# Kernel tuning notes

Measured on AMD Instinct MI355X. Metric: run time of the kernel, lower is better.

## Reference

```python
import jax, jax.numpy as jnp
import numpy as np

MARGIN = 0.3
EPS = 1e-6  # torch TripletMarginLoss pairwise_distance eps


def setup_inputs() -> dict:
    key = jax.random.key(0)
    k1, k2 = jax.random.split(key)
    n, d = 8192, 128
    inputs = jax.random.normal(k1, (n, d), dtype=jnp.float32)
    similarity = jax.random.randint(k2, (n, n), 0, 2, dtype=jnp.int32)
    return {"inputs": inputs, "similarity": similarity}


def reference(inputs, similarity):
    # mask[i, j] = True if j is a positive of anchor i
    mask = similarity != 0                      # (n, n) bool
    maskf = mask.astype(inputs.dtype)
    counts = maskf.sum(axis=1, keepdims=True)   # (n, 1), >0 by construction
    # per-anchor center = mean of its positives (masked mean as a GEMM)
    centers = (maskf @ inputs) / counts         # (n, d)
    # dist[i, j] = ||centers[i] - inputs[j]||_2 via the expansion trick
    # (avoids materializing the (n, n, d) difference tensor of the original)
    c2 = jnp.sum(centers * centers, axis=1)[:, None]
    x2 = jnp.sum(inputs * inputs, axis=1)[None, :]
    d2 = c2 + x2 - 2.0 * (centers @ inputs.T)
    dist = jnp.sqrt(jnp.maximum(d2, 0.0))       # (n, n)
    # dist only feeds argmin in the original (indices carry no grad)
    dist = jax.lax.stop_gradient(dist)
    # hard-negative mining: argmin of dist over negatives of each anchor
    neg_idx = jnp.argmin(jnp.where(mask, jnp.inf, dist), axis=1)  # (n,)
    neg_min = inputs[neg_idx]                   # (n, d)
    # TripletMarginLoss(margin=0.3, p=2): anchor=centers, pos=inputs, neg=neg_min
    d_ap = jnp.linalg.norm(centers - inputs + EPS, axis=1)
    d_an = jnp.linalg.norm(centers - neg_min + EPS, axis=1)
    return jnp.mean(jnp.maximum(d_ap - d_an + MARGIN, 0.0))
```

## Files before the change

kernel.cpp:

```cpp
#include <hip/hip_runtime.h>
#include <stdint.h>

#define NN 8192
#define DD 128

typedef float f32x4 __attribute__((ext_vector_type(4)));
typedef short bf16x8 __attribute__((ext_vector_type(8)));

union B8 { uint32_t u[4]; bf16x8 v; };

__device__ inline uint16_t f2bf(float f) {
  uint32_t u = __builtin_bit_cast(uint32_t, f);
  uint32_t r = (u + 0x7FFFu + ((u >> 16) & 1u)) >> 16;
  return (uint16_t)r;
}

__device__ inline f32x4 mfma16(bf16x8 a, bf16x8 b, f32x4 c) {
  return __builtin_amdgcn_mfma_f32_16x16x32_bf16(a, b, c, 0, 0, 0);
}

__global__ __launch_bounds__(256) void k_prep(const float* __restrict__ inp,
                                              uint16_t* __restrict__ inp_bf,
                                              uint16_t* __restrict__ inpT_bf,
                                              float* __restrict__ x2) {
  __shared__ uint16_t ldsT[128 * 65];
  __shared__ float ldsS[256];
  const int tid = threadIdx.x;
  const int j0 = blockIdx.x * 64;
  const int r = tid >> 2;
  const int dseg = (tid & 3) * 32;
  float ss = 0.f;
#pragma unroll
  for (int it = 0; it < 8; ++it) {
    float4 v = *(const float4*)(inp + (size_t)(j0 + r) * DD + dseg + it * 4);
    ss += v.x * v.x + v.y * v.y + v.z * v.z + v.w * v.w;
    uint16_t b0 = f2bf(v.x), b1 = f2bf(v.y), b2 = f2bf(v.z), b3 = f2bf(v.w);
    *(ushort4*)(inp_bf + (size_t)(j0 + r) * DD + dseg + it * 4) = make_ushort4(b0, b1, b2, b3);
    int d = dseg + it * 4;
    ldsT[(d + 0) * 65 + r] = b0;
    ldsT[(d + 1) * 65 + r] = b1;
    ldsT[(d + 2) * 65 + r] = b2;
    ldsT[(d + 3) * 65 + r] = b3;
  }
  ldsS[tid] = ss;
  __syncthreads();
  if (tid < 64) x2[j0 + tid] = ldsS[tid * 4] + ldsS[tid * 4 + 1] + ldsS[tid * 4 + 2] + ldsS[tid * 4 + 3];
#pragma unroll
  for (int it = 0; it < 32; ++it) {
    int flat = it * 256 + tid;
    int d = flat >> 6, jl = flat & 63;
    inpT_bf[(size_t)d * NN + j0 + jl] = ldsT[d * 65 + jl];
  }
}

__global__ __launch_bounds__(256) void k_bitgen(const int* __restrict__ sim,
                                                uint32_t* __restrict__ bmT,
                                                uint32_t* __restrict__ counts) {
  __shared__ uint32_t ldsW[64 * 64];
  const int tid = threadIdx.x, lane = tid & 63, w = tid >> 6;
  const int m0 = blockIdx.x * 64;
  const int c0 = blockIdx.y * 2048;
#pragma unroll 1
  for (int rr = 0; rr < 16; ++rr) {
    const int rl = rr * 4 + w;
    const int row = m0 + rl;
    const int* p = sim + (size_t)row * NN + c0 + lane;
    int v[32];
#pragma unroll
    for (int s = 0; s < 32; ++s) v[s] = p[s * 64];
    uint32_t cnt = 0;
#pragma unroll
    for (int s = 0; s < 32; ++s) {
      unsigned long long ball = __ballot(v[s] != 0);
      cnt += (uint32_t)__popcll(ball);
      if ((lane & 31) == 0)
        ldsW[(s * 2 + (lane >> 5)) * 64 + rl] = (uint32_t)(ball >> (lane & 32));
    }
    if (lane == 0) atomicAdd(&counts[row], cnt);
  }
  __syncthreads();
#pragma unroll
  for (int it = 0; it < 16; ++it) {
    int idx = it * 256 + tid;
    int kw = idx >> 6, r = idx & 63;
    bmT[(size_t)((c0 >> 5) + kw) * NN + m0 + r] = ldsW[idx];
  }
}

__global__ __launch_bounds__(512) void k_gemm1(const uint16_t* __restrict__ inpT,
                                               const uint32_t* __restrict__ bmT,
                                               float* __restrict__ part) {
  __shared__ __align__(16) uint16_t ldsB[128 * 40];
  __shared__ uint32_t ldsM[128];
  const int tid = threadIdx.x, lane = tid & 63, w = tid >> 6;
  const int col = lane & 15, quad = lane >> 4;
  const int m0 = blockIdx.x * 128;
  const int kb0 = blockIdx.y * 2048;
  const int wm = (w >> 1) * 32, wn = (w & 1) * 64;
  const int dim = tid >> 2, koff = (tid & 3) * 8;
  f32x4 acc[2][4];
  const f32x4 z = {0.f, 0.f, 0.f, 0.f};
#pragma unroll
  for (int r = 0; r < 2; ++r)
#pragma unroll
    for (int c = 0; c < 4; ++c) acc[r][c] = z;

  bf16x8 bpf = *(const bf16x8*)(inpT + (size_t)dim * NN + kb0 + koff);
  uint32_t mpf = (tid < 128) ? bmT[(size_t)(kb0 >> 5) * NN + m0 + tid] : 0u;

  for (int ks = 0; ks < 64; ++ks) {
    const int kb = kb0 + ks * 32;
    __syncthreads();
    *(bf16x8*)(ldsB + dim * 40 + koff) = bpf;
    if (tid < 128) ldsM[tid] = mpf;
    __syncthreads();
    if (ks < 63) {
      bpf = *(const bf16x8*)(inpT + (size_t)dim * NN + kb + 32 + koff);
      if (tid < 128) mpf = bmT[(size_t)((kb + 32) >> 5) * NN + m0 + tid];
    }
    B8 af[2];
#pragma unroll
    for (int rr = 0; rr < 2; ++rr) {
      uint32_t word = ldsM[wm + rr * 16 + col];
      uint32_t b = (word >> (quad * 8)) & 0xFFu;
      uint32_t s = b * 0x8001u;
#pragma unroll
      for (int p = 0; p < 4; ++p) {
        uint32_t t = (s >> (2 * p)) & 0x10001u;
        af[rr].u[p] = t * 0x3F80u;
      }
    }
#pragma unroll
    for (int cc = 0; cc < 4; ++cc) {
      bf16x8 bfr = *(const bf16x8*)(ldsB + (wn + cc * 16 + col) * 40 + quad * 8);
#pragma unroll
      for (int rr = 0; rr < 2; ++rr) acc[rr][cc] = mfma16(af[rr].v, bfr, acc[rr][cc]);
    }
  }
  float* pp = part + (size_t)blockIdx.y * NN * DD;
#pragma unroll
  for (int rr = 0; rr < 2; ++rr)
#pragma unroll
    for (int cc = 0; cc < 4; ++cc)
#pragma unroll
      for (int g = 0; g < 4; ++g)
        pp[(size_t)(m0 + wm + rr * 16 + quad * 4 + g) * DD + wn + cc * 16 + col] = acc[rr][cc][g];
}

__global__ __launch_bounds__(256) void k_reduce(const float* __restrict__ part,
                                                const uint32_t* __restrict__ counts,
                                                float* __restrict__ centers,
                                                uint16_t* __restrict__ cen_bf,
                                                unsigned long long* __restrict__ negkey) {
  const int gid = blockIdx.x * 256 + threadIdx.x;
  if (gid < NN) negkey[gid] = ~0ull;
  const int idx = gid * 4;
  const int row = idx >> 7;
  const float inv = 1.0f / (float)counts[row];
  float4 v = *(const float4*)(part + idx);
#pragma unroll
  for (int s = 1; s < 4; ++s) {
    float4 u = *(const float4*)(part + (size_t)s * NN * DD + idx);
    v.x += u.x; v.y += u.y; v.z += u.z; v.w += u.w;
  }
  v.x *= inv; v.y *= inv; v.z *= inv; v.w *= inv;
  *(float4*)(centers + idx) = v;
  *(ushort4*)(cen_bf + idx) = make_ushort4(f2bf(v.x), f2bf(v.y), f2bf(v.z), f2bf(v.w));
}

__global__ __launch_bounds__(256) void k_argmin(const uint16_t* __restrict__ cen_bf,
                                                const uint16_t* __restrict__ inp_bf,
                                                const uint32_t* __restrict__ bmT,
                                                const float* __restrict__ x2,
                                                unsigned long long* __restrict__ negkey) {
  __shared__ __align__(16) uint16_t ldsB[64 * 136];
  __shared__ uint32_t ldsM[128];
  __shared__ float ldsX[64];
  __shared__ unsigned long long ldsR[64];
  const int tid = threadIdx.x, lane = tid & 63, w = tid >> 6;
  const int col = lane & 15, quad = lane >> 4;
  const int i0 = blockIdx.x * 64;
  const int jbase = blockIdx.y * 2048;
  const int wi = (w >> 1) * 32, wj = (w & 1) * 32;
  bf16x8 af[2][4];
#pragma unroll
  for (int rr = 0; rr < 2; ++rr)
#pragma unroll
    for (int kk = 0; kk < 4; ++kk)
      af[rr][kk] = *(const bf16x8*)(cen_bf + (size_t)(i0 + wi + rr * 16 + col) * DD + kk * 32 + quad * 8);
  if (tid < 64) ldsR[tid] = ~0ull;
  float bestv[2][4];
  uint32_t besti[2][4];
#pragma unroll
  for (int rr = 0; rr < 2; ++rr)
#pragma unroll
    for (int g = 0; g < 4; ++g) { bestv[rr][g] = __builtin_inff(); besti[rr][g] = 0u; }

  const int jl = tid >> 2, doff = (tid & 3) * 32;
  bf16x8 bpf[4];
#pragma unroll
  for (int it = 0; it < 4; ++it)
    bpf[it] = *(const bf16x8*)(inp_bf + (size_t)(jbase + jl) * DD + doff + it * 8);
  uint32_t mpf = (tid < 128) ? bmT[(size_t)((jbase >> 5) + (tid >> 6)) * NN + i0 + (tid & 63)] : 0u;
  float xpf = (tid >= 128 && tid < 192) ? x2[jbase + tid - 128] : 0.f;

  for (int js = 0; js < 32; ++js) {
    const int j0 = jbase + js * 64;
    __syncthreads();
#pragma unroll
    for (int it = 0; it < 4; ++it)
      *(bf16x8*)(ldsB + jl * 136 + doff + it * 8) = bpf[it];
    if (tid < 128) ldsM[tid] = mpf;
    else if (tid < 192) ldsX[tid - 128] = xpf;
    __syncthreads();
    if (js < 31) {
#pragma unroll
      for (int it = 0; it < 4; ++it)
        bpf[it] = *(const bf16x8*)(inp_bf + (size_t)(j0 + 64 + jl) * DD + doff + it * 8);
      if (tid < 128) mpf = bmT[(size_t)(((j0 + 64) >> 5) + (tid >> 6)) * NN + i0 + (tid & 63)];
      else if (tid < 192) xpf = x2[j0 + 64 + tid - 128];
    }
    f32x4 acc[2][2];
    const f32x4 z = {0.f, 0.f, 0.f, 0.f};
    acc[0][0] = z; acc[0][1] = z; acc[1][0] = z; acc[1][1] = z;
#pragma unroll
    for (int kk = 0; kk < 4; ++kk) {
      bf16x8 b0 = *(const bf16x8*)(ldsB + (wj + col) * 136 + kk * 32 + quad * 8);
      bf16x8 b1 = *(const bf16x8*)(ldsB + (wj + 16 + col) * 136 + kk * 32 + quad * 8);
      acc[0][0] = mfma16(af[0][kk], b0, acc[0][0]);
      acc[0][1] = mfma16(af[0][kk], b1, acc[0][1]);
      acc[1][0] = mfma16(af[1][kk], b0, acc[1][0]);
      acc[1][1] = mfma16(af[1][kk], b1, acc[1][1]);
    }
    uint32_t wsel = (w & 1) * 64;
    uint32_t words[2][4];
#pragma unroll
    for (int rr = 0; rr < 2; ++rr)
#pragma unroll
      for (int g = 0; g < 4; ++g) words[rr][g] = ldsM[wsel + wi + rr * 16 + quad * 4 + g];
#pragma unroll
    for (int cc = 0; cc < 2; ++cc) {
      const int jj = wj + cc * 16 + col;
      const float xq = ldsX[jj];
      const uint32_t jg = (uint32_t)(j0 + jj);
      const uint32_t bit = cc * 16 + col;
#pragma unroll
      for (int rr = 0; rr < 2; ++rr)
#pragma unroll
        for (int g = 0; g < 4; ++g) {
          float v = fmaf(-2.0f, acc[rr][cc][g], xq);
          if ((words[rr][g] >> bit) & 1u) v = __builtin_inff();
          if (v < bestv[rr][g]) { bestv[rr][g] = v; besti[rr][g] = jg; }
        }
    }
  }
#pragma unroll
  for (int rr = 0; rr < 2; ++rr)
#pragma unroll
    for (int g = 0; g < 4; ++g) {
      float v = bestv[rr][g];
      uint32_t ix = besti[rr][g];
#pragma unroll
      for (int d = 1; d < 16; d <<= 1) {
        float ov = __shfl_xor(v, d);
        uint32_t oi = (uint32_t)__shfl_xor((int)ix, d);
        if (ov < v || (ov == v && oi < ix)) { v = ov; ix = oi; }
      }
      if (col == 0) {
        uint32_t vb = __builtin_bit_cast(uint32_t, v);
        uint32_t key32 = (vb & 0x80000000u) ? ~vb : (vb | 0x80000000u);
        unsigned long long key = ((unsigned long long)key32 << 32) | (unsigned long long)ix;
        atomicMin(&ldsR[wi + rr * 16 + quad * 4 + g], key);
      }
    }
  __syncthreads();
  if (tid < 64) atomicMin(&negkey[i0 + tid], ldsR[tid]);
}

__global__ __launch_bounds__(256) void k_loss(const float* __restrict__ centers,
                                              const float* __restrict__ inp,
                                              const unsigned long long* __restrict__ negkey,
                                              float* __restrict__ out) {
  __shared__ float lds[4];
  const int tid = threadIdx.x, lane = tid & 63, w = tid >> 6;
  float local = 0.f;
#pragma unroll 1
  for (int a = 0; a < 4; ++a) {
    int i = blockIdx.x * 16 + w * 4 + a;
    float2 c = *(const float2*)(centers + (size_t)i * DD + lane * 2);
    float2 x = *(const float2*)(inp + (size_t)i * DD + lane * 2);
    uint32_t ni = ((uint32_t)(negkey[i] & 0xFFFFFFFFull)) & (NN - 1);
    float2 gv = *(const float2*)(inp + (size_t)ni * DD + lane * 2);
    float e0 = c.x - x.x + 1e-6f, e1 = c.y - x.y + 1e-6f;
    float f0 = c.x - gv.x + 1e-6f, f1 = c.y - gv.y + 1e-6f;
    float dap = e0 * e0 + e1 * e1;
    float dan = f0 * f0 + f1 * f1;
#pragma unroll
    for (int d = 32; d; d >>= 1) {
      dap += __shfl_down(dap, d);
      dan += __shfl_down(dan, d);
    }
    if (lane == 0) local += fmaxf(sqrtf(dap) - sqrtf(dan) + 0.3f, 0.f);
  }
  if (lane == 0) lds[w] = local;
  __syncthreads();
  if (tid == 0) atomicAdd(out, (lds[0] + lds[1] + lds[2] + lds[3]) * (1.0f / 8192.0f));
}

extern "C" void kernel_launch(void* const* d_in, const int* in_sizes, int n_in,
                              void* d_out, int out_size, void* d_ws, size_t ws_size,
                              hipStream_t stream) {
  (void)in_sizes; (void)n_in; (void)ws_size;
  const float* inp = (const float*)d_in[0];
  const int* sim = (const int*)d_in[1];
  float* out = (float*)d_out;
  char* ws = (char*)d_ws;

  uint32_t* bmT     = (uint32_t*)ws;
  float* part       = (float*)(ws + (8u << 20));
  float* centers    = (float*)(ws + (24u << 20));
  uint16_t* inp_bf  = (uint16_t*)(ws + (28u << 20));
  uint16_t* inpT_bf = (uint16_t*)(ws + (30u << 20));
  uint16_t* cen_bf  = (uint16_t*)(ws + (32u << 20));
  float* x2         = (float*)(ws + (34u << 20));
  uint32_t* counts  = (uint32_t*)(ws + (34u << 20) + 32768u);
  unsigned long long* negkey = (unsigned long long*)(ws + (34u << 20) + 65536u);

  hipMemsetAsync(counts, 0, NN * sizeof(uint32_t), stream);
  hipMemsetAsync(out, 0, out_size * sizeof(float), stream);

  k_prep<<<128, 256, 0, stream>>>(inp, inp_bf, inpT_bf, x2);
  k_bitgen<<<dim3(128, 4), 256, 0, stream>>>(sim, bmT, counts);
  k_gemm1<<<dim3(64, 4), 512, 0, stream>>>(inpT_bf, bmT, part);
  k_reduce<<<1024, 256, 0, stream>>>(part, counts, centers, cen_bf, negkey);
  k_argmin<<<dim3(128, 4), 256, 0, stream>>>(cen_bf, inp_bf, bmT, x2, negkey);
  k_loss<<<512, 256, 0, stream>>>(centers, inp, negkey, out);
}
```

Baseline: 455.2 us.

## Pack argmin into 32-bit keys and double split-K grids

The argmin inner loop now forms a single 32-bit key: the float distance biased positive by 512, with low mantissa bits replaced by the column index and the mask bit forced into the sign. A plain unsigned min then replaces the compare/select pairs, and the 64-bit shuffles and atomics become 32-bit. Both GEMM kernels double their grid by halving K/J chunks (8 partials, 256-thread blocks), which adds occupancy but also more partial-sum traffic in the reduce. The key truncates 13 mantissa bits of the distance, so near-ties can choose a different negative than exact argmin.

```diff
diff --git a/kernel.cpp b/kernel.cpp
--- a/kernel.cpp
+++ b/kernel.cpp
@@ -22,7 +22,7 @@
 __global__ __launch_bounds__(256) void k_prep(const float* __restrict__ inp,
                                               uint16_t* __restrict__ inp_bf,
                                               uint16_t* __restrict__ inpT_bf,
-                                              float* __restrict__ x2) {
+                                              float* __restrict__ x2p) {
   __shared__ uint16_t ldsT[128 * 65];
   __shared__ float ldsS[256];
   const int tid = threadIdx.x;
@@ -44,7 +44,8 @@
   }
   ldsS[tid] = ss;
   __syncthreads();
-  if (tid < 64) x2[j0 + tid] = ldsS[tid * 4] + ldsS[tid * 4 + 1] + ldsS[tid * 4 + 2] + ldsS[tid * 4 + 3];
+  if (tid < 64)
+    x2p[j0 + tid] = ldsS[tid * 4] + ldsS[tid * 4 + 1] + ldsS[tid * 4 + 2] + ldsS[tid * 4 + 3] + 512.0f;
 #pragma unroll
   for (int it = 0; it < 32; ++it) {
     int flat = it * 256 + tid;
@@ -87,17 +88,17 @@
   }
 }
 
-__global__ __launch_bounds__(512) void k_gemm1(const uint16_t* __restrict__ inpT,
-                                               const uint32_t* __restrict__ bmT,
-                                               float* __restrict__ part) {
+__global__ __launch_bounds__(256, 4) void k_gemm1(const uint16_t* __restrict__ inpT,
+                                                  const uint32_t* __restrict__ bmT,
+                                                  float* __restrict__ part) {
   __shared__ __align__(16) uint16_t ldsB[128 * 40];
-  __shared__ uint32_t ldsM[128];
+  __shared__ uint32_t ldsM[64];
   const int tid = threadIdx.x, lane = tid & 63, w = tid >> 6;
   const int col = lane & 15, quad = lane >> 4;
-  const int m0 = blockIdx.x * 128;
-  const int kb0 = blockIdx.y * 2048;
+  const int m0 = blockIdx.x * 64;
+  const int kb0 = blockIdx.y * 1024;
   const int wm = (w >> 1) * 32, wn = (w & 1) * 64;
-  const int dim = tid >> 2, koff = (tid & 3) * 8;
+  const int dim = tid >> 1, koff = (tid & 1) * 16;
   f32x4 acc[2][4];
   const f32x4 z = {0.f, 0.f, 0.f, 0.f};
 #pragma unroll
@@ -105,18 +106,21 @@
 #pragma unroll
     for (int c = 0; c < 4; ++c) acc[r][c] = z;
 
-  bf16x8 bpf = *(const bf16x8*)(inpT + (size_t)dim * NN + kb0 + koff);
-  uint32_t mpf = (tid < 128) ? bmT[(size_t)(kb0 >> 5) * NN + m0 + tid] : 0u;
-
-  for (int ks = 0; ks < 64; ++ks) {
+  bf16x8 bpf0 = *(const bf16x8*)(inpT + (size_t)dim * NN + kb0 + koff);
+  bf16x8 bpf1 = *(const bf16x8*)(inpT + (size_t)dim * NN + kb0 + koff + 8);
+  uint32_t mpf = (tid < 64) ? bmT[(size_t)(kb0 >> 5) * NN + m0 + tid] : 0u;
+
+  for (int ks = 0; ks < 32; ++ks) {
     const int kb = kb0 + ks * 32;
     __syncthreads();
-    *(bf16x8*)(ldsB + dim * 40 + koff) = bpf;
-    if (tid < 128) ldsM[tid] = mpf;
+    *(bf16x8*)(ldsB + dim * 40 + koff) = bpf0;
+    *(bf16x8*)(ldsB + dim * 40 + koff + 8) = bpf1;
+    if (tid < 64) ldsM[tid] = mpf;
     __syncthreads();
-    if (ks < 63) {
-      bpf = *(const bf16x8*)(inpT + (size_t)dim * NN + kb + 32 + koff);
-      if (tid < 128) mpf = bmT[(size_t)((kb + 32) >> 5) * NN + m0 + tid];
+    if (ks < 31) {
+      bpf0 = *(const bf16x8*)(inpT + (size_t)dim * NN + kb + 32 + koff);
+      bpf1 = *(const bf16x8*)(inpT + (size_t)dim * NN + kb + 32 + koff + 8);
+      if (tid < 64) mpf = bmT[(size_t)((kb + 32) >> 5) * NN + m0 + tid];
     }
     B8 af[2];
 #pragma unroll
@@ -150,16 +154,14 @@
 __global__ __launch_bounds__(256) void k_reduce(const float* __restrict__ part,
                                                 const uint32_t* __restrict__ counts,
                                                 float* __restrict__ centers,
-                                                uint16_t* __restrict__ cen_bf,
-                                                unsigned long long* __restrict__ negkey) {
+                                                uint16_t* __restrict__ cen_bf) {
   const int gid = blockIdx.x * 256 + threadIdx.x;
-  if (gid < NN) negkey[gid] = ~0ull;
   const int idx = gid * 4;
   const int row = idx >> 7;
   const float inv = 1.0f / (float)counts[row];
   float4 v = *(const float4*)(part + idx);
 #pragma unroll
-  for (int s = 1; s < 4; ++s) {
+  for (int s = 1; s < 8; ++s) {
     float4 u = *(const float4*)(part + (size_t)s * NN * DD + idx);
     v.x += u.x; v.y += u.y; v.z += u.z; v.w += u.w;
   }
@@ -168,19 +170,19 @@
   *(ushort4*)(cen_bf + idx) = make_ushort4(f2bf(v.x), f2bf(v.y), f2bf(v.z), f2bf(v.w));
 }
 
-__global__ __launch_bounds__(256) void k_argmin(const uint16_t* __restrict__ cen_bf,
-                                                const uint16_t* __restrict__ inp_bf,
-                                                const uint32_t* __restrict__ bmT,
-                                                const float* __restrict__ x2,
-                                                unsigned long long* __restrict__ negkey) {
+__global__ __launch_bounds__(256, 4) void k_argmin(const uint16_t* __restrict__ cen_bf,
+                                                   const uint16_t* __restrict__ inp_bf,
+                                                   const uint32_t* __restrict__ bmT,
+                                                   const float* __restrict__ x2p,
+                                                   uint32_t* __restrict__ negkey) {
   __shared__ __align__(16) uint16_t ldsB[64 * 136];
   __shared__ uint32_t ldsM[128];
   __shared__ float ldsX[64];
-  __shared__ unsigned long long ldsR[64];
+  __shared__ uint32_t ldsR[64];
   const int tid = threadIdx.x, lane = tid & 63, w = tid >> 6;
   const int col = lane & 15, quad = lane >> 4;
   const int i0 = blockIdx.x * 64;
-  const int jbase = blockIdx.y * 2048;
+  const int jbase = blockIdx.y * 1024;
   const int wi = (w >> 1) * 32, wj = (w & 1) * 32;
   bf16x8 af[2][4];
 #pragma unroll
@@ -188,13 +190,12 @@
 #pragma unroll
     for (int kk = 0; kk < 4; ++kk)
       af[rr][kk] = *(const bf16x8*)(cen_bf + (size_t)(i0 + wi + rr * 16 + col) * DD + kk * 32 + quad * 8);
-  if (tid < 64) ldsR[tid] = ~0ull;
-  float bestv[2][4];
-  uint32_t besti[2][4];
+  if (tid < 64) ldsR[tid] = 0xFFFFFFFFu;
+  uint32_t best[2][4];
 #pragma unroll
   for (int rr = 0; rr < 2; ++rr)
 #pragma unroll
-    for (int g = 0; g < 4; ++g) { bestv[rr][g] = __builtin_inff(); besti[rr][g] = 0u; }
+    for (int g = 0; g < 4; ++g) best[rr][g] = 0xFFFFFFFFu;
 
   const int jl = tid >> 2, doff = (tid & 3) * 32;
   bf16x8 bpf[4];
@@ -202,9 +203,9 @@
   for (int it = 0; it < 4; ++it)
     bpf[it] = *(const bf16x8*)(inp_bf + (size_t)(jbase + jl) * DD + doff + it * 8);
   uint32_t mpf = (tid < 128) ? bmT[(size_t)((jbase >> 5) + (tid >> 6)) * NN + i0 + (tid & 63)] : 0u;
-  float xpf = (tid >= 128 && tid < 192) ? x2[jbase + tid - 128] : 0.f;
-
-  for (int js = 0; js < 32; ++js) {
+  float xpf = (tid >= 128 && tid < 192) ? x2p[jbase + tid - 128] : 0.f;
+
+  for (int js = 0; js < 16; ++js) {
     const int j0 = jbase + js * 64;
     __syncthreads();
 #pragma unroll
@@ -213,12 +214,12 @@
     if (tid < 128) ldsM[tid] = mpf;
     else if (tid < 192) ldsX[tid - 128] = xpf;
     __syncthreads();
-    if (js < 31) {
+    if (js < 15) {
 #pragma unroll
       for (int it = 0; it < 4; ++it)
         bpf[it] = *(const bf16x8*)(inp_bf + (size_t)(j0 + 64 + jl) * DD + doff + it * 8);
       if (tid < 128) mpf = bmT[(size_t)(((j0 + 64) >> 5) + (tid >> 6)) * NN + i0 + (tid & 63)];
-      else if (tid < 192) xpf = x2[j0 + 64 + tid - 128];
+      else if (tid < 192) xpf = x2p[j0 + 64 + tid - 128];
     }
     f32x4 acc[2][2];
     const f32x4 z = {0.f, 0.f, 0.f, 0.f};
@@ -232,7 +233,7 @@
       acc[1][0] = mfma16(af[1][kk], b0, acc[1][0]);
       acc[1][1] = mfma16(af[1][kk], b1, acc[1][1]);
     }
-    uint32_t wsel = (w & 1) * 64;
+    const uint32_t wsel = (w & 1) * 64;
     uint32_t words[2][4];
 #pragma unroll
     for (int rr = 0; rr < 2; ++rr)
@@ -242,15 +243,17 @@
     for (int cc = 0; cc < 2; ++cc) {
       const int jj = wj + cc * 16 + col;
       const float xq = ldsX[jj];
-      const uint32_t jg = (uint32_t)(j0 + jj);
-      const uint32_t bit = cc * 16 + col;
+      const uint32_t jpre = (uint32_t)(j0 + jj);
+      const int sh = 31 - (cc * 16 + col);
 #pragma unroll
       for (int rr = 0; rr < 2; ++rr)
 #pragma unroll
         for (int g = 0; g < 4; ++g) {
           float v = fmaf(-2.0f, acc[rr][cc][g], xq);
-          if ((words[rr][g] >> bit) & 1u) v = __builtin_inff();
-          if (v < bestv[rr][g]) { bestv[rr][g] = v; besti[rr][g] = jg; }
+          uint32_t u = __builtin_bit_cast(uint32_t, v);
+          uint32_t key = (u & 0xFFFFE000u) | jpre;
+          key |= (words[rr][g] << sh) & 0x80000000u;
+          best[rr][g] = min(best[rr][g], key);
         }
     }
   }
@@ -258,20 +261,13 @@
   for (int rr = 0; rr < 2; ++rr)
 #pragma unroll
     for (int g = 0; g < 4; ++g) {
-      float v = bestv[rr][g];
-      uint32_t ix = besti[rr][g];
+      uint32_t k = best[rr][g];
 #pragma unroll
       for (int d = 1; d < 16; d <<= 1) {
-        float ov = __shfl_xor(v, d);
-        uint32_t oi = (uint32_t)__shfl_xor((int)ix, d);
-        if (ov < v || (ov == v && oi < ix)) { v = ov; ix = oi; }
+        uint32_t o = (uint32_t)__shfl_xor((int)k, d);
+        k = min(k, o);
       }
-      if (col == 0) {
-        uint32_t vb = __builtin_bit_cast(uint32_t, v);
-        uint32_t key32 = (vb & 0x80000000u) ? ~vb : (vb | 0x80000000u);
-        unsigned long long key = ((unsigned long long)key32 << 32) | (unsigned long long)ix;
-        atomicMin(&ldsR[wi + rr * 16 + quad * 4 + g], key);
-      }
+      if (col == 0) atomicMin(&ldsR[wi + rr * 16 + quad * 4 + g], k);
     }
   __syncthreads();
   if (tid < 64) atomicMin(&negkey[i0 + tid], ldsR[tid]);
@@ -279,7 +275,7 @@
 
 __global__ __launch_bounds__(256) void k_loss(const float* __restrict__ centers,
                                               const float* __restrict__ inp,
-                                              const unsigned long long* __restrict__ negkey,
+                                              const uint32_t* __restrict__ negkey,
                                               float* __restrict__ out) {
   __shared__ float lds[4];
   const int tid = threadIdx.x, lane = tid & 63, w = tid >> 6;
@@ -289,7 +285,7 @@
     int i = blockIdx.x * 16 + w * 4 + a;
     float2 c = *(const float2*)(centers + (size_t)i * DD + lane * 2);
     float2 x = *(const float2*)(inp + (size_t)i * DD + lane * 2);
-    uint32_t ni = ((uint32_t)(negkey[i] & 0xFFFFFFFFull)) & (NN - 1);
+    uint32_t ni = negkey[i] & (NN - 1);
     float2 gv = *(const float2*)(inp + (size_t)ni * DD + lane * 2);
     float e0 = c.x - x.x + 1e-6f, e1 = c.y - x.y + 1e-6f;
     float f0 = c.x - gv.x + 1e-6f, f1 = c.y - gv.y + 1e-6f;
@@ -318,21 +314,22 @@
 
   uint32_t* bmT     = (uint32_t*)ws;
   float* part       = (float*)(ws + (8u << 20));
-  float* centers    = (float*)(ws + (24u << 20));
-  uint16_t* inp_bf  = (uint16_t*)(ws + (28u << 20));
-  uint16_t* inpT_bf = (uint16_t*)(ws + (30u << 20));
-  uint16_t* cen_bf  = (uint16_t*)(ws + (32u << 20));
-  float* x2         = (float*)(ws + (34u << 20));
-  uint32_t* counts  = (uint32_t*)(ws + (34u << 20) + 32768u);
-  unsigned long long* negkey = (unsigned long long*)(ws + (34u << 20) + 65536u);
+  float* centers    = (float*)(ws + (40u << 20));
+  uint16_t* inp_bf  = (uint16_t*)(ws + (44u << 20));
+  uint16_t* inpT_bf = (uint16_t*)(ws + (46u << 20));
+  uint16_t* cen_bf  = (uint16_t*)(ws + (48u << 20));
+  float* x2p        = (float*)(ws + (50u << 20));
+  uint32_t* counts  = (uint32_t*)(ws + (50u << 20) + 32768u);
+  uint32_t* negkey  = (uint32_t*)(ws + (50u << 20) + 65536u);
 
   hipMemsetAsync(counts, 0, NN * sizeof(uint32_t), stream);
+  hipMemsetAsync(negkey, 0xFF, NN * sizeof(uint32_t), stream);
   hipMemsetAsync(out, 0, out_size * sizeof(float), stream);
 
-  k_prep<<<128, 256, 0, stream>>>(inp, inp_bf, inpT_bf, x2);
+  k_prep<<<128, 256, 0, stream>>>(inp, inp_bf, inpT_bf, x2p);
   k_bitgen<<<dim3(128, 4), 256, 0, stream>>>(sim, bmT, counts);
-  k_gemm1<<<dim3(64, 4), 512, 0, stream>>>(inpT_bf, bmT, part);
-  k_reduce<<<1024, 256, 0, stream>>>(part, counts, centers, cen_bf, negkey);
-  k_argmin<<<dim3(128, 4), 256, 0, stream>>>(cen_bf, inp_bf, bmT, x2, negkey);
+  k_gemm1<<<dim3(128, 8), 256, 0, stream>>>(inpT_bf, bmT, part);
+  k_reduce<<<1024, 256, 0, stream>>>(part, counts, centers, cen_bf);
+  k_argmin<<<dim3(128, 8), 256, 0, stream>>>(cen_bf, inp_bf, bmT, x2p, negkey);
   k_loss<<<512, 256, 0, stream>>>(centers, inp, negkey, out);
 }
```

After: 451.6 us. No clear change (-0.8%).
